# Kernel tuning notes

Hardware: AMD Instinct MI355X
Metric: run time of the kernel (lower is better)

Reference implementation:

```python
import jax, jax.numpy as jnp
import numpy as np

LAYERS = 16
F_SAMPLES = 48   # frequency (pilot subcarrier) samples
T_SAMPLES = 512  # time-domain samples


def dft_matrices(F=F_SAMPLES, T=T_SAMPLES):
    # IDFT: [F, T] maps freq-domain [B,F] -> time-domain [B,T]
    # DFT:  [T, F] maps time-domain [B,T] -> freq-domain [B,F]
    f = np.arange(F)[:, None]
    t = np.arange(T)[None, :]
    ang = 2.0 * np.pi * f * t / T                      # [F, T]
    scale = 1.0 / np.sqrt(T)
    idft_re = jnp.asarray(np.cos(ang) * scale, jnp.float32)   # [F, T]
    idft_im = jnp.asarray(np.sin(ang) * scale, jnp.float32)
    dft_re = jnp.asarray(np.cos(ang).T * scale, jnp.float32)  # [T, F]
    dft_im = jnp.asarray(-np.sin(ang).T * scale, jnp.float32)
    return dft_re, dft_im, idft_re, idft_im


def mm(a_re, a_im, b_re, b_im):
    # complex matmul (a_re + i a_im) @ (b_re + i b_im) via 4 real GEMMs
    return (a_re @ b_re - a_im @ b_im,
            a_re @ b_im + a_im @ b_re)


def soft_gate(x, s1, s2):
    # sigmoid(x, S1, S2) = logistic(S1 * (x - S2)) -- soft-threshold gate
    return jax.nn.sigmoid(s1 * (x - s2))


def setup_inputs() -> dict:
    key = jax.random.key(0)
    u = jax.random.normal(key, (16384, F_SAMPLES, 2), dtype=jnp.float32)
    S1 = jnp.full((1,), 10.0, dtype=jnp.float32)
    S2 = jnp.full((1,), 0.5, dtype=jnp.float32)
    return {"u": u, "S1": S1, "S2": S2}


def reference(u, S1, S2):
    dft_re, dft_im, idft_re, idft_im = dft_matrices()
    B = u.shape[0]

    maximum = jnp.abs(u.max())
    u = 5.0 * u / maximum
    u_re, u_im = u[:, :, 0], u[:, :, 1]

    z_re, z_im = u_re, u_im
    H_re = jnp.zeros((B, T_SAMPLES), jnp.float32)
    H_im = jnp.zeros((B, T_SAMPLES), jnp.float32)

    def layer(carry, _):
        z_re, z_im, H_re, H_im = carry
        Z_re, Z_im = mm(z_re, z_im, idft_re, idft_im)      # [B, T]
        R_re = H_re + Z_re
        R_im = H_im + Z_im
        R_mean = jnp.sqrt(jnp.mean(R_re * R_re + R_im * R_im, axis=0))  # [T]
        g = soft_gate(R_mean, S1[0], S2[0])                # [T]
        H_re = R_re * g
        H_im = R_im * g
        h_re, h_im = mm(H_re, H_im, dft_re, dft_im)        # [B, F]
        z_re = u_re - h_re
        z_im = u_im - h_im
        return (z_re, z_im, H_re, H_im), None

    (z_re, z_im, H_re, H_im), _ = jax.lax.scan(
        layer, (z_re, z_im, H_re, H_im), None, length=LAYERS)

    h_re, h_im = mm(H_re, H_im, dft_re, dft_im)            # [B, F]
    out = jnp.stack((h_re, h_im), axis=2)                  # [B, F, 2]
    out = out / 5.0 * maximum
    return out
```

## Files before the change

### kernel.cpp

```cpp
#include <hip/hip_runtime.h>
#include <math.h>

#define NROWS 16384
#define FC 96
#define T 512
#define NRI 1024
#define LAYERS 16
#define NBLK 256

typedef _Float16 f16;
typedef _Float16 half8 __attribute__((ext_vector_type(8)));
typedef _Float16 half4 __attribute__((ext_vector_type(4)));
typedef float floatx4 __attribute__((ext_vector_type(4)));

#define OFF_MAXKEY 0
#define OFF_ARR  64
#define OFF_REL  (OFF_ARR + NBLK * 32)
#define OFF_W1   (OFF_REL + NBLK * 32)
#define OFF_W1L  (OFF_W1 + 49152)
#define OFF_W2   (OFF_W1L + 49152)
#define OFF_W2L  (OFF_W2 + 49152)
#define OFF_PART (OFF_W2L + 49152)
#define OFF_FIN  (OFF_PART + NBLK * NRI)

#define SMEM_BYTES 155648

__global__ void ksetup(float* __restrict__ ws) {
    int t = threadIdx.x;
    if (t == 0)
        __hip_atomic_store((unsigned*)(ws + OFF_MAXKEY), 0u, __ATOMIC_RELAXED, __HIP_MEMORY_SCOPE_AGENT);
    for (int i = t; i < 2 * NBLK * 32; i += 256)
        __hip_atomic_store((unsigned*)(ws + OFF_ARR) + i, 0u, __ATOMIC_RELAXED, __HIP_MEMORY_SCOPE_AGENT);
}

__global__ void kwf(float* __restrict__ ws) {
    int idx = blockIdx.x * 256 + threadIdx.x;
    if (idx >= 2 * 98304) return;
    int which = idx >= 98304;
    int id = which ? idx - 98304 : idx;
    int j = id & 7, lane = (id >> 3) & 63, rem = id >> 9;
    int k, n;
    if (!which) { int kc = rem % 3,  nt = rem / 3;  k = kc*32 + (lane>>4)*8 + j; n = nt*16 + (lane&15); }
    else        { int kc = rem & 31, nt = rem >> 5; k = kc*32 + (lane>>4)*8 + j; n = nt*16 + (lane&15); }
    int t, f, q, e;
    if (!which) { t = n >> 1; e = n & 1; f = k >> 1; q = k & 1; }
    else        { t = k >> 1; q = k & 1; f = n >> 1; e = n & 1; }
    int ft = (f * t) & (T - 1);
    float sv, cv;
    sincosf((float)ft * 0.012271846303085129f, &sv, &cv);
    const float sc = 0.04419417382415922f;
    cv *= sc; sv *= sc;
    float val;
    if (!which) val = (e == 0) ? (q == 0 ? cv : -sv) : (q == 0 ?  sv : cv);
    else        val = (e == 0) ? (q == 0 ? cv :  sv) : (q == 0 ? -sv : cv);
    f16 hi = (f16)val;
    f16 lo = (f16)(val - (float)hi);
    f16* H = (f16*)(ws + (which ? OFF_W2 : OFF_W1));
    f16* L = (f16*)(ws + (which ? OFF_W2L : OFF_W1L));
    H[id] = hi;
    L[id] = lo;
}

__device__ __forceinline__ void gbar2(float* __restrict__ ws, unsigned e) {
    asm volatile("s_waitcnt vmcnt(0)" ::: "memory");
    __syncthreads();
    const int tid = threadIdx.x;
    unsigned* __restrict__ Af = (unsigned*)(ws + OFF_ARR);
    unsigned* __restrict__ Rf = (unsigned*)(ws + OFF_REL);
    if (blockIdx.x == 0) {
        if (tid < 64) {
            bool ok;
            do {
                __builtin_amdgcn_s_sleep(1);
                ok = true;
#pragma unroll
                for (int s = 0; s < NBLK / 64; s++) {
                    int b = s * 64 + tid;
                    unsigned v = __hip_atomic_load(&Af[b * 32], __ATOMIC_RELAXED, __HIP_MEMORY_SCOPE_AGENT);
                    ok = ok && (b == 0 || v >= e);
                }
            } while (!__all(ok));
            asm volatile("" ::: "memory");
#pragma unroll
            for (int s = 0; s < NBLK / 64; s++) {
                int b = s * 64 + tid;
                __hip_atomic_store(&Rf[b * 32], e, __ATOMIC_RELAXED, __HIP_MEMORY_SCOPE_AGENT);
            }
        }
        __syncthreads();
    } else {
        if (tid == 0) {
            __hip_atomic_store(&Af[blockIdx.x * 32], e, __ATOMIC_RELAXED, __HIP_MEMORY_SCOPE_AGENT);
            while (__hip_atomic_load(&Rf[blockIdx.x * 32], __ATOMIC_RELAXED, __HIP_MEMORY_SCOPE_AGENT) < e)
                __builtin_amdgcn_s_sleep(2);
            asm volatile("" ::: "memory");
        }
        __syncthreads();
    }
}

__device__ __forceinline__ void coh_store8(float* p, float a, float b) {
    unsigned long long v = ((unsigned long long)__float_as_uint(b) << 32) | __float_as_uint(a);
    (void)__hip_atomic_exchange((unsigned long long*)p, v, __ATOMIC_RELAXED, __HIP_MEMORY_SCOPE_AGENT);
}

__global__ __launch_bounds__(512, 2) void kmain(const float* __restrict__ u,
                                                const float* __restrict__ S1,
                                                const float* __restrict__ S2,
                                                float* __restrict__ out,
                                                float* __restrict__ ws) {
    extern __shared__ char smem[];
    f16* zh = (f16*)smem;
    f16* zl = zh + 64 * FC;
    f16* Hs = zl + 64 * FC;
    __shared__ float smax[8];

    const int tid = threadIdx.x;
    const int w = tid >> 6;
    const int lane = tid & 63;
    const int q = lane >> 4;
    const int l15 = lane & 15;
    const int row0 = blockIdx.x * 64;
    const float s1 = S1[0], s2 = S2[0];

    unsigned epoch = 1;

    float m = -1e30f;
    for (int i = tid; i < 64 * FC; i += 512) m = fmaxf(m, u[(long)row0 * FC + i]);
#pragma unroll
    for (int s = 1; s < 64; s <<= 1) m = fmaxf(m, __shfl_xor(m, s, 64));
    if (lane == 0) smax[w] = m;
    __syncthreads();
    if (tid == 0) {
        float mm = smax[0];
#pragma unroll
        for (int i = 1; i < 8; i++) mm = fmaxf(mm, smax[i]);
        unsigned k = __float_as_uint(mm);
        k = (k & 0x80000000u) ? ~k : (k | 0x80000000u);
        atomicMax((unsigned*)(ws + OFF_MAXKEY), k);
    }
    gbar2(ws, epoch); epoch++;
    unsigned key = __hip_atomic_load((unsigned*)(ws + OFF_MAXKEY), __ATOMIC_RELAXED, __HIP_MEMORY_SCOPE_AGENT);
    unsigned ku = (key & 0x80000000u) ? (key ^ 0x80000000u) : ~key;
    const float gmax = fabsf(__uint_as_float(ku));
    const float sc_to = 5.0f / gmax;
    const float sc_from = gmax / 5.0f;

    for (int i = tid; i < 64 * FC; i += 512) {
        int b = i / FC, fc = i - b * FC;
        float z = sc_to * u[(long)row0 * FC + i];
        f16 h = (f16)z;
        int idx = b * FC + ((fc & ~31) | ((fc & 31) ^ ((b & 3) << 3)));
        zh[idx] = h;
        zl[idx] = (f16)(z - (float)h);
    }

    floatx4 R[32];
#pragma unroll
    for (int i = 0; i < 32; i++) R[i] = (floatx4){0.f, 0.f, 0.f, 0.f};

    const f16* __restrict__ w1h = (const f16*)(ws + OFF_W1);
    const f16* __restrict__ w1l = (const f16*)(ws + OFF_W1L);
    const f16* __restrict__ w2h = (const f16*)(ws + OFF_W2);
    const f16* __restrict__ w2l = (const f16*)(ws + OFF_W2L);

    const int brow = (w & 3) * 16 + l15;
    const int fh = (w >> 2) * 3;
    const int aswz = (brow & 7) << 3;
    const long hrow = (long)brow * NRI;

    float gcur = 0.0f;

#pragma unroll 1
    for (int l = 0; l < LAYERS; l++) {
        __syncthreads();

        if (l > 0) {
#pragma unroll
            for (int ntl = 0; ntl < 8; ntl++) {
                float ga = __shfl(gcur, ntl * 8 + q * 2, 64);
                float gb = __shfl(gcur, ntl * 8 + q * 2 + 1, 64);
#pragma unroll
                for (int bt = 0; bt < 4; bt++) {
                    R[ntl * 4 + bt][0] *= ga;
                    R[ntl * 4 + bt][1] *= ga;
                    R[ntl * 4 + bt][2] *= gb;
                    R[ntl * 4 + bt][3] *= gb;
                }
            }
        }
#pragma unroll
        for (int kc = 0; kc < 3; kc++) {
            half8 Bh[4], Bl[4];
#pragma unroll
            for (int bt = 0; bt < 4; bt++) {
                int b = bt * 16 + l15;
                int zi = b * FC + kc * 32 + ((q ^ (b & 3)) << 3);
                Bh[bt] = *(const half8*)(zh + zi);
                Bl[bt] = *(const half8*)(zl + zi);
            }
#pragma unroll
            for (int ntl = 0; ntl < 8; ntl++) {
                int wi = (((w * 8 + ntl) * 3 + kc) * 64 + lane) * 8;
                half8 Ah = *(const half8*)(w1h + wi);
                half8 Al = *(const half8*)(w1l + wi);
#pragma unroll
                for (int bt = 0; bt < 4; bt++) {
                    R[ntl*4+bt] = __builtin_amdgcn_mfma_f32_16x16x32_f16(Ah, Bh[bt], R[ntl*4+bt], 0, 0, 0);
                    R[ntl*4+bt] = __builtin_amdgcn_mfma_f32_16x16x32_f16(Ah, Bl[bt], R[ntl*4+bt], 0, 0, 0);
                    R[ntl*4+bt] = __builtin_amdgcn_mfma_f32_16x16x32_f16(Al, Bh[bt], R[ntl*4+bt], 0, 0, 0);
                }
            }
        }

        {
            float* part = ws + OFF_PART + (long)blockIdx.x * NRI;
#pragma unroll
            for (int ntl = 0; ntl < 8; ntl++) {
                floatx4 ps;
#pragma unroll
                for (int r = 0; r < 4; r++) {
                    float p = R[ntl*4+0][r] * R[ntl*4+0][r];
                    p = fmaf(R[ntl*4+1][r], R[ntl*4+1][r], p);
                    p = fmaf(R[ntl*4+2][r], R[ntl*4+2][r], p);
                    p = fmaf(R[ntl*4+3][r], R[ntl*4+3][r], p);
                    p += __shfl_xor(p, 1, 64);
                    p += __shfl_xor(p, 2, 64);
                    p += __shfl_xor(p, 4, 64);
                    p += __shfl_xor(p, 8, 64);
                    ps[r] = p;
                }
                if (l15 == 0) {
                    int n = w * 128 + ntl * 16 + q * 4;
                    coh_store8(part + n, ps[0], ps[1]);
                    coh_store8(part + n + 2, ps[2], ps[3]);
                }
            }
        }
        gbar2(ws, epoch); epoch++;

        if (w == 0) {
            const int n0 = blockIdx.x * 4;
            const float* pb = ws + OFF_PART;
            floatx4 cs = {0.f, 0.f, 0.f, 0.f};
#pragma unroll
            for (int s4 = 0; s4 < 4; s4++) {
                long off = (long)(s4 * 64 + lane) * NRI + n0;
                unsigned long long a = __hip_atomic_load((const unsigned long long*)(pb + off),
                                                         __ATOMIC_RELAXED, __HIP_MEMORY_SCOPE_AGENT);
                unsigned long long b = __hip_atomic_load((const unsigned long long*)(pb + off + 2),
                                                         __ATOMIC_RELAXED, __HIP_MEMORY_SCOPE_AGENT);
                cs[0] += __uint_as_float((unsigned)a);
                cs[1] += __uint_as_float((unsigned)(a >> 32));
                cs[2] += __uint_as_float((unsigned)b);
                cs[3] += __uint_as_float((unsigned)(b >> 32));
            }
#pragma unroll
            for (int sh = 1; sh < 64; sh <<= 1) {
                cs[0] += __shfl_xor(cs[0], sh, 64);
                cs[1] += __shfl_xor(cs[1], sh, 64);
                cs[2] += __shfl_xor(cs[2], sh, 64);
                cs[3] += __shfl_xor(cs[3], sh, 64);
            }
            if (lane == 0) {
                coh_store8(ws + OFF_FIN + n0, cs[0], cs[1]);
                coh_store8(ws + OFF_FIN + n0 + 2, cs[2], cs[3]);
            }
        }
        gbar2(ws, epoch); epoch++;

        {
            int n = w * 128 + lane * 2;
            unsigned long long pv = __hip_atomic_load((const unsigned long long*)(ws + OFF_FIN + n),
                                                      __ATOMIC_RELAXED, __HIP_MEMORY_SCOPE_AGENT);
            float sa = __uint_as_float((unsigned)pv);
            float sb = __uint_as_float((unsigned)(pv >> 32));
            float rm = sqrtf((sa + sb) * (1.0f / 16384.0f));
            gcur = 1.0f / (1.0f + expf(-s1 * (rm - s2)));
        }

#pragma unroll
        for (int ntl = 0; ntl < 8; ntl++) {
            float ga = __shfl(gcur, ntl * 8 + q * 2, 64);
            float gb = __shfl(gcur, ntl * 8 + q * 2 + 1, 64);
            floatx4 g4 = {ga, ga, gb, gb};
            int col = w * 128 + ntl * 16 + q * 4;
#pragma unroll
            for (int bt = 0; bt < 4; bt++) {
                int row = bt * 16 + l15;
                half4 vh;
#pragma unroll
                for (int r = 0; r < 4; r++) vh[r] = (f16)(g4[r] * R[ntl * 4 + bt][r]);
                *(half4*)(Hs + row * NRI + (col ^ ((row & 7) << 3))) = vh;
            }
        }
        __syncthreads();

        floatx4 acc[3];
#pragma unroll
        for (int i = 0; i < 3; i++) acc[i] = (floatx4){0.f, 0.f, 0.f, 0.f};
#pragma unroll 4
        for (int kg = 0; kg < 32; kg++) {
            half8 Ah = *(const half8*)(Hs + hrow + ((kg * 32 + q * 8) ^ aswz));
#pragma unroll
            for (int ft = 0; ft < 3; ft++) {
                int wi = (((fh + ft) * 32 + kg) * 64 + lane) * 8;
                half8 Wh = *(const half8*)(w2h + wi);
                half8 Wl = *(const half8*)(w2l + wi);
                acc[ft] = __builtin_amdgcn_mfma_f32_16x16x32_f16(Ah, Wh, acc[ft], 0, 0, 0);
                acc[ft] = __builtin_amdgcn_mfma_f32_16x16x32_f16(Ah, Wl, acc[ft], 0, 0, 0);
            }
        }

        if (l < LAYERS - 1) {
#pragma unroll
            for (int ft = 0; ft < 3; ft++) {
                int fcg = (fh + ft) * 16 + l15;
#pragma unroll
                for (int r = 0; r < 4; r++) {
                    int b = (w & 3) * 16 + q * 4 + r;
                    float z = fmaf(sc_to, u[(long)(row0 + b) * FC + fcg], -acc[ft][r]);
                    f16 h = (f16)z;
                    int idx = b * FC + ((fcg & ~31) | ((fcg & 31) ^ ((b & 3) << 3)));
                    zh[idx] = h;
                    zl[idx] = (f16)(z - (float)h);
                }
            }
        } else {
#pragma unroll
            for (int ft = 0; ft < 3; ft++) {
                int fcg = (fh + ft) * 16 + l15;
#pragma unroll
                for (int r = 0; r < 4; r++) {
                    int b = (w & 3) * 16 + q * 4 + r;
                    out[(long)(row0 + b) * FC + fcg] = acc[ft][r] * sc_from;
                }
            }
        }
    }
}

extern "C" void kernel_launch(void* const* d_in, const int* in_sizes, int n_in,
                              void* d_out, int out_size, void* d_ws, size_t ws_size,
                              hipStream_t stream) {
    (void)in_sizes; (void)n_in; (void)out_size; (void)ws_size;
    const float* u  = (const float*)d_in[0];
    const float* S1 = (const float*)d_in[1];
    const float* S2 = (const float*)d_in[2];
    float* out = (float*)d_out;
    float* ws  = (float*)d_ws;

    static int inited = 0;
    if (!inited) {
        hipFuncSetAttribute((const void*)kmain, hipFuncAttributeMaxDynamicSharedMemorySize, SMEM_BYTES);
        inited = 1;
    }

    ksetup<<<1, 256, 0, stream>>>(ws);
    kwf<<<768, 256, 0, stream>>>(ws);

    void* args[] = {(void*)&u, (void*)&S1, (void*)&S2, (void*)&out, (void*)&ws};
    hipLaunchCooperativeKernel((const void*)kmain, dim3(NBLK), dim3(512), args,
                               (unsigned)SMEM_BYTES, stream);
}
```

Before: 1.251 ms.

## Restructure cross-block partial-sum reduction with pair-major layout and vector coherent loads

Combines the re and im partial energies per time sample before publishing, halving the partial buffer. The buffer is laid out pair-major so each block's reducer reads its column with two dwordx4 loads instead of many scattered 64-bit atomic loads. The final sums are fetched once by one wave into shared memory rather than by every thread with atomics. Atomic exchanges are replaced by sc0 sc1 inline-asm stores and loads, which shortens the critical path between the grid barriers. It relies on the cache-coherence bits in hand-written asm being correct.

After: 1.297 ms. +3.7%, slower.

```diff
diff --git a/kernel.cpp b/kernel.cpp
--- a/kernel.cpp
+++ b/kernel.cpp
@@ -5,6 +5,7 @@
 #define FC 96
 #define T 512
 #define NRI 1024
+#define NPAIR 512
 #define LAYERS 16
 #define NBLK 256
 
@@ -12,6 +13,7 @@
 typedef _Float16 half8 __attribute__((ext_vector_type(8)));
 typedef _Float16 half4 __attribute__((ext_vector_type(4)));
 typedef float floatx4 __attribute__((ext_vector_type(4)));
+typedef float floatx2 __attribute__((ext_vector_type(2)));
 
 #define OFF_MAXKEY 0
 #define OFF_ARR  64
@@ -21,9 +23,9 @@
 #define OFF_W2   (OFF_W1L + 49152)
 #define OFF_W2L  (OFF_W2 + 49152)
 #define OFF_PART (OFF_W2L + 49152)
-#define OFF_FIN  (OFF_PART + NBLK * NRI)
-
-#define SMEM_BYTES 155648
+#define OFF_FIN  (OFF_PART + NPAIR * NBLK)
+
+#define SMEM_BYTES 157696
 
 __global__ void ksetup(float* __restrict__ ws) {
     int t = threadIdx.x;
@@ -99,9 +101,20 @@
     }
 }
 
-__device__ __forceinline__ void coh_store8(float* p, float a, float b) {
-    unsigned long long v = ((unsigned long long)__float_as_uint(b) << 32) | __float_as_uint(a);
-    (void)__hip_atomic_exchange((unsigned long long*)p, v, __ATOMIC_RELAXED, __HIP_MEMORY_SCOPE_AGENT);
+__device__ __forceinline__ void coh_store4(float* p, float v) {
+    asm volatile("global_store_dword %0, %1, off sc0 sc1" :: "v"(p), "v"(v) : "memory");
+}
+__device__ __forceinline__ void coh_store8v(float* p, floatx2 v) {
+    asm volatile("global_store_dwordx2 %0, %1, off sc0 sc1" :: "v"(p), "v"(v) : "memory");
+}
+__device__ __forceinline__ void coh_load2x16(const float* pa, const float* pb,
+                                             floatx4& va, floatx4& vb) {
+    asm volatile("global_load_dwordx4 %0, %2, off sc0 sc1\n\t"
+                 "global_load_dwordx4 %1, %3, off sc0 sc1\n\t"
+                 "s_waitcnt vmcnt(0)"
+                 : "=&v"(va), "=&v"(vb)
+                 : "v"(pa), "v"(pb)
+                 : "memory");
 }
 
 __global__ __launch_bounds__(512, 2) void kmain(const float* __restrict__ u,
@@ -113,6 +126,7 @@
     f16* zh = (f16*)smem;
     f16* zl = zh + 64 * FC;
     f16* Hs = zl + 64 * FC;
+    float* garr = (float*)(Hs + 64 * NRI);
     __shared__ float smax[8];
 
     const int tid = threadIdx.x;
@@ -163,6 +177,8 @@
     const f16* __restrict__ w1l = (const f16*)(ws + OFF_W1L);
     const f16* __restrict__ w2h = (const f16*)(ws + OFF_W2);
     const f16* __restrict__ w2l = (const f16*)(ws + OFF_W2L);
+    float* __restrict__ partP = ws + OFF_PART;
+    float* __restrict__ fin = ws + OFF_FIN;
 
     const int brow = (w & 3) * 16 + l15;
     const int fh = (w >> 2) * 3;
@@ -213,69 +229,55 @@
             }
         }
 
+#pragma unroll
+        for (int ntl = 0; ntl < 8; ntl++) {
+            floatx4 ps;
+#pragma unroll
+            for (int r = 0; r < 4; r++) {
+                float p = R[ntl*4+0][r] * R[ntl*4+0][r];
+                p = fmaf(R[ntl*4+1][r], R[ntl*4+1][r], p);
+                p = fmaf(R[ntl*4+2][r], R[ntl*4+2][r], p);
+                p = fmaf(R[ntl*4+3][r], R[ntl*4+3][r], p);
+                p += __shfl_xor(p, 1, 64);
+                p += __shfl_xor(p, 2, 64);
+                p += __shfl_xor(p, 4, 64);
+                p += __shfl_xor(p, 8, 64);
+                ps[r] = p;
+            }
+            if (l15 == 0) {
+                int p0 = w * 64 + ntl * 8 + q * 2;
+                coh_store4(partP + p0 * NBLK + blockIdx.x, ps[0] + ps[1]);
+                coh_store4(partP + (p0 + 1) * NBLK + blockIdx.x, ps[2] + ps[3]);
+            }
+        }
+        gbar2(ws, epoch); epoch++;
+
+        if (w == 0) {
+            const float* pa = partP + (2 * blockIdx.x) * NBLK + 4 * lane;
+            const float* pb = partP + (2 * blockIdx.x + 1) * NBLK + 4 * lane;
+            floatx4 va, vb;
+            coh_load2x16(pa, pb, va, vb);
+            float c0 = va[0] + va[1] + va[2] + va[3];
+            float c1 = vb[0] + vb[1] + vb[2] + vb[3];
+#pragma unroll
+            for (int sh = 1; sh < 64; sh <<= 1) {
+                c0 += __shfl_xor(c0, sh, 64);
+                c1 += __shfl_xor(c1, sh, 64);
+            }
+            if (lane == 0) coh_store8v(fin + 2 * blockIdx.x, (floatx2){c0, c1});
+        }
+        gbar2(ws, epoch); epoch++;
+
+        if (w == 0) {
+            floatx4 va, vb;
+            coh_load2x16(fin + 4 * lane, fin + 256 + 4 * lane, va, vb);
+            *(floatx4*)(garr + 4 * lane) = va;
+            *(floatx4*)(garr + 256 + 4 * lane) = vb;
+        }
+        __syncthreads();
         {
-            float* part = ws + OFF_PART + (long)blockIdx.x * NRI;
-#pragma unroll
-            for (int ntl = 0; ntl < 8; ntl++) {
-                floatx4 ps;
-#pragma unroll
-                for (int r = 0; r < 4; r++) {
-                    float p = R[ntl*4+0][r] * R[ntl*4+0][r];
-                    p = fmaf(R[ntl*4+1][r], R[ntl*4+1][r], p);
-                    p = fmaf(R[ntl*4+2][r], R[ntl*4+2][r], p);
-                    p = fmaf(R[ntl*4+3][r], R[ntl*4+3][r], p);
-                    p += __shfl_xor(p, 1, 64);
-                    p += __shfl_xor(p, 2, 64);
-                    p += __shfl_xor(p, 4, 64);
-                    p += __shfl_xor(p, 8, 64);
-                    ps[r] = p;
-                }
-                if (l15 == 0) {
-                    int n = w * 128 + ntl * 16 + q * 4;
-                    coh_store8(part + n, ps[0], ps[1]);
-                    coh_store8(part + n + 2, ps[2], ps[3]);
-                }
-            }
-        }
-        gbar2(ws, epoch); epoch++;
-
-        if (w == 0) {
-            const int n0 = blockIdx.x * 4;
-            const float* pb = ws + OFF_PART;
-            floatx4 cs = {0.f, 0.f, 0.f, 0.f};
-#pragma unroll
-            for (int s4 = 0; s4 < 4; s4++) {
-                long off = (long)(s4 * 64 + lane) * NRI + n0;
-                unsigned long long a = __hip_atomic_load((const unsigned long long*)(pb + off),
-                                                         __ATOMIC_RELAXED, __HIP_MEMORY_SCOPE_AGENT);
-                unsigned long long b = __hip_atomic_load((const unsigned long long*)(pb + off + 2),
-                                                         __ATOMIC_RELAXED, __HIP_MEMORY_SCOPE_AGENT);
-                cs[0] += __uint_as_float((unsigned)a);
-                cs[1] += __uint_as_float((unsigned)(a >> 32));
-                cs[2] += __uint_as_float((unsigned)b);
-                cs[3] += __uint_as_float((unsigned)(b >> 32));
-            }
-#pragma unroll
-            for (int sh = 1; sh < 64; sh <<= 1) {
-                cs[0] += __shfl_xor(cs[0], sh, 64);
-                cs[1] += __shfl_xor(cs[1], sh, 64);
-                cs[2] += __shfl_xor(cs[2], sh, 64);
-                cs[3] += __shfl_xor(cs[3], sh, 64);
-            }
-            if (lane == 0) {
-                coh_store8(ws + OFF_FIN + n0, cs[0], cs[1]);
-                coh_store8(ws + OFF_FIN + n0 + 2, cs[2], cs[3]);
-            }
-        }
-        gbar2(ws, epoch); epoch++;
-
-        {
-            int n = w * 128 + lane * 2;
-            unsigned long long pv = __hip_atomic_load((const unsigned long long*)(ws + OFF_FIN + n),
-                                                      __ATOMIC_RELAXED, __HIP_MEMORY_SCOPE_AGENT);
-            float sa = __uint_as_float((unsigned)pv);
-            float sb = __uint_as_float((unsigned)(pv >> 32));
-            float rm = sqrtf((sa + sb) * (1.0f / 16384.0f));
+            float sum = garr[w * 64 + lane];
+            float rm = sqrtf(sum * (1.0f / 16384.0f));
             gcur = 1.0f / (1.0f + expf(-s1 * (rm - s2)));
         }
 
```
